# Optimization experiments

Hardware: AMD Instinct MI355X
Metric: run time of the kernel (lower is better)

The kernel has to match this reference:

```python
import jax, jax.numpy as jnp
import numpy as np

NUM_HEADS = 8
WINDOW = 128  # num_previous_frames
EPS = 1e-5


def setup_inputs() -> dict:
    key = jax.random.key(0)
    ks = jax.random.split(key, 5)
    B, T, E = 8, 1024, 512
    x = jax.random.normal(ks[0], (B, T, E), dtype=jnp.float32)
    x_lengths = jax.random.randint(ks[1], (B,), 1, T + 1).astype(jnp.int32)
    gamma = jnp.ones((E,), dtype=jnp.float32)
    beta = jnp.zeros((E,), dtype=jnp.float32)
    sc_in = 1.0 / np.sqrt(E)
    w_in = jax.random.normal(ks[2], (3 * E, E), dtype=jnp.float32) * sc_in
    b_in = jnp.zeros((3 * E,), dtype=jnp.float32)
    w_out = jax.random.normal(ks[3], (E, E), dtype=jnp.float32) * sc_in
    b_out = jnp.zeros((E,), dtype=jnp.float32)
    return {"x": x, "x_lengths": x_lengths, "gamma": gamma, "beta": beta,
            "w_in": w_in, "b_in": b_in, "w_out": w_out, "b_out": b_out}


def _forward(x, gamma, beta, w_in, b_in, w_out, b_out):
    B, T, E = x.shape
    H = NUM_HEADS
    D = E // H
    # Timewise LayerNorm: normalize over channel dim per (batch, time)
    mu = jnp.mean(x, axis=-1, keepdims=True)
    var = jnp.mean(jnp.square(x - mu), axis=-1, keepdims=True)
    xn = (x - mu) * jax.lax.rsqrt(var + EPS) * gamma + beta
    # in-projection: qkv packed
    qkv = xn @ w_in.T + b_in  # [B,T,3E]
    q, k, v = jnp.split(qkv, 3, axis=-1)
    q = q.reshape(B, T, H, D)
    k = k.reshape(B, T, H, D)
    v = v.reshape(B, T, H, D)
    scale = 1.0 / np.sqrt(D)
    scores = jnp.einsum('bqhd,bkhd->bhqk', q * scale, k)  # [B,H,T,T]
    # banded causal mask: allow j in [i-WINDOW, i]
    i = jnp.arange(T)[:, None]
    j = jnp.arange(T)[None, :]
    allowed = (j <= i) & (j >= i - WINDOW)
    scores = jnp.where(allowed[None, None], scores, -jnp.inf)
    attn = jax.nn.softmax(scores, axis=-1)
    ctx = jnp.einsum('bhqk,bkhd->bqhd', attn, v).reshape(B, T, E)
    out = ctx @ w_out.T + b_out
    return out  # dropout is identity in eval mode


def reference(x, x_lengths, gamma, beta, w_in, b_in, w_out, b_out):
    del x_lengths  # unused by the original forward (no key_padding_mask passed)
    return _forward(x, gamma, beta, w_in, b_in, w_out, b_out)
```

## Files before the change

kernel.cpp:

```cpp
#include <hip/hip_runtime.h>
#include <stdint.h>

typedef __bf16 bf16;
typedef __bf16 bf16x4 __attribute__((ext_vector_type(4)));
typedef __bf16 bf16x8 __attribute__((ext_vector_type(8)));
typedef float f32x4 __attribute__((ext_vector_type(4)));

#define MFMA_16x16x32(a, b, c) __builtin_amdgcn_mfma_f32_16x16x32_bf16((a), (b), (c), 0, 0, 0)

__device__ __forceinline__ void gl_lds16(const bf16* g, bf16* l) {
    __builtin_amdgcn_global_load_lds(
        (const __attribute__((address_space(1))) void*)g,
        (__attribute__((address_space(3))) void*)l, 16, 0, 0);
}

__global__ __launch_bounds__(256) void prep_kernel(const float* __restrict__ x,
                                                   const float* __restrict__ gamma,
                                                   const float* __restrict__ beta,
                                                   const float* __restrict__ w_in,
                                                   const float* __restrict__ w_out,
                                                   bf16* __restrict__ xn,
                                                   bf16* __restrict__ cw_in,
                                                   bf16* __restrict__ cw_out) {
    const int bid = blockIdx.x;
    if (bid < 2048) {
        const int lane = threadIdx.x & 63;
        const int row = (bid << 2) + (threadIdx.x >> 6);
        const size_t base = (size_t)row * 512 + lane * 8;
        const float* xf = x + base;
        float4 a = *(const float4*)xf;
        float4 b = *(const float4*)(xf + 4);
        float f[8] = {a.x, a.y, a.z, a.w, b.x, b.y, b.z, b.w};
        float s = 0.f;
#pragma unroll
        for (int j = 0; j < 8; ++j) s += f[j];
#pragma unroll
        for (int off = 32; off >= 1; off >>= 1) s += __shfl_xor(s, off, 64);
        const float mu = s * (1.0f / 512.0f);
        float vs = 0.f;
#pragma unroll
        for (int j = 0; j < 8; ++j) { float d = f[j] - mu; vs += d * d; }
#pragma unroll
        for (int off = 32; off >= 1; off >>= 1) vs += __shfl_xor(vs, off, 64);
        const float rstd = rsqrtf(vs * (1.0f / 512.0f) + 1e-5f);
        float4 g0 = *(const float4*)(gamma + lane * 8);
        float4 g1 = *(const float4*)(gamma + lane * 8 + 4);
        float4 b0 = *(const float4*)(beta + lane * 8);
        float4 b1 = *(const float4*)(beta + lane * 8 + 4);
        float gg[8] = {g0.x, g0.y, g0.z, g0.w, g1.x, g1.y, g1.z, g1.w};
        float bb[8] = {b0.x, b0.y, b0.z, b0.w, b1.x, b1.y, b1.z, b1.w};
        bf16x8 o;
#pragma unroll
        for (int j = 0; j < 8; ++j)
            o[j] = (bf16)((f[j] - mu) * rstd * gg[j] + bb[j]);
        *(bf16x8*)(xn + base) = o;
    } else {
        const float* src;
        bf16* dst;
        int base;
        if (bid < 2432) { src = w_in;  dst = cw_in;  base = (bid - 2048) * 2048; }
        else            { src = w_out; dst = cw_out; base = (bid - 2432) * 2048; }
        const int i = base + threadIdx.x * 8;
        float4 a = *(const float4*)(src + i);
        float4 b = *(const float4*)(src + i + 4);
        float f[8] = {a.x, a.y, a.z, a.w, b.x, b.y, b.z, b.w};
        bf16x8 o;
#pragma unroll
        for (int j = 0; j < 8; ++j) o[j] = (bf16)f[j];
        *(bf16x8*)(dst + i) = o;
    }
}

template <int TM, typename OT>
__global__ __launch_bounds__(256) void gemm_bt(const bf16* __restrict__ A,
                                               const bf16* __restrict__ B,
                                               const float* __restrict__ bias,
                                               OT* __restrict__ C,
                                               int N, int K) {
    constexpr int MI = TM / 32;
    constexpr int NCA = TM * 8;
    __shared__ alignas(16) bf16 As[TM * 64];
    __shared__ alignas(16) bf16 Bs[128 * 64];
    const int tid = threadIdx.x;
    const int lane = tid & 63;
    const int wid = tid >> 6;
    const int wm = (wid >> 1) * (TM / 2), wn = (wid & 1) * 64;
    const int m0 = blockIdx.y * TM, n0 = blockIdx.x * 128;
    const int l15 = lane & 15, l16 = lane >> 4;

    f32x4 acc[MI][4] = {};

    const bf16* Abase = A + (size_t)m0 * K;
    const bf16* Bbase = B + (size_t)n0 * K;

    for (int k0 = 0; k0 < K; k0 += 64) {
#pragma unroll
        for (int c = tid; c < NCA; c += 256) {
            const int p = c / (TM * 4);
            const int r = (c % (TM * 4)) >> 2;
            const int ko = (c & 3) * 8 + p * 32;
            gl_lds16(Abase + (size_t)r * K + k0 + ko, &As[c * 8]);
        }
#pragma unroll
        for (int c = tid; c < 1024; c += 256) {
            const int p = c >> 9;
            const int r = (c & 511) >> 2;
            const int ko = (c & 3) * 8 + p * 32;
            gl_lds16(Bbase + (size_t)r * K + k0 + ko, &Bs[c * 8]);
        }
        __syncthreads();
#pragma unroll
        for (int h = 0; h < 2; ++h) {
            bf16x8 af[MI], bfr[4];
#pragma unroll
            for (int t = 0; t < MI; ++t)
                af[t] = *(const bf16x8*)&As[h * (TM * 32) + (wm + t * 16 + l15) * 32 + l16 * 8];
#pragma unroll
            for (int t = 0; t < 4; ++t)
                bfr[t] = *(const bf16x8*)&Bs[h * 4096 + (wn + t * 16 + l15) * 32 + l16 * 8];
#pragma unroll
            for (int i = 0; i < MI; ++i)
#pragma unroll
                for (int j = 0; j < 4; ++j)
                    acc[i][j] = MFMA_16x16x32(bfr[j], af[i], acc[i][j]);
        }
        __syncthreads();
    }

#pragma unroll
    for (int j = 0; j < 4; ++j) {
        const int colb = n0 + wn + j * 16 + (l16 << 2);
        const float4 bv = *(const float4*)(bias + colb);
#pragma unroll
        for (int i = 0; i < MI; ++i) {
            const int row = m0 + wm + i * 16 + l15;
            if constexpr (sizeof(OT) == 2) {
                bf16x4 o;
                o[0] = (bf16)(acc[i][j][0] + bv.x);
                o[1] = (bf16)(acc[i][j][1] + bv.y);
                o[2] = (bf16)(acc[i][j][2] + bv.z);
                o[3] = (bf16)(acc[i][j][3] + bv.w);
                *(bf16x4*)&C[(size_t)row * N + colb] = o;
            } else {
                float4 o;
                o.x = acc[i][j][0] + bv.x;
                o.y = acc[i][j][1] + bv.y;
                o.z = acc[i][j][2] + bv.z;
                o.w = acc[i][j][3] + bv.w;
                *(float4*)&C[(size_t)row * N + colb] = o;
            }
        }
    }
}

#define KS_STRIDE 72
#define PW_STRIDE 72
#define VT_ROWB 400

__global__ __launch_bounds__(256) void attn_kernel(const bf16* __restrict__ qkv,
                                                   bf16* __restrict__ ctx) {
    __shared__ alignas(16) bf16 Ks[192 * KS_STRIDE];
    __shared__ alignas(16) char Vt[64 * VT_ROWB];
    __shared__ alignas(16) bf16 Pbuf[4 * 16 * PW_STRIDE];

    const int tid = threadIdx.x;
    const int lane = tid & 63, wid = tid >> 6;
    const int l15 = lane & 15, l16 = lane >> 4;
    const int bid = blockIdx.y * 16 + blockIdx.x;
    const int swz = (bid & 7) * 128 + (bid >> 3);
    const int bh = swz >> 4, b = bh >> 3, h = bh & 7;
    const int q0 = (swz & 15) * 64;
    const int kv0 = (q0 > 128) ? (q0 - 128) : 0;
    const int nk = q0 + 64 - kv0;
    const size_t tokbase = (size_t)b * 1024;

    for (int c = tid; c < nk * 8; c += 256) {
        const int kk = c >> 3, dc = (c & 7) * 8;
        const bf16* src = qkv + (tokbase + kv0 + kk) * 1536 + h * 64 + dc + 512;
        *(uint4*)&Ks[kk * KS_STRIDE + dc] = *(const uint4*)src;
    }
    for (int c = tid; c < nk * 4; c += 256) {
        const int kp = c >> 3, dc = (c & 7) * 8;
        const bf16* s0 = qkv + (tokbase + kv0 + 2 * kp) * 1536 + h * 64 + dc + 1024;
        uint4 w0 = *(const uint4*)s0;
        uint4 w1 = *(const uint4*)(s0 + 1536);
        const unsigned short* a0 = (const unsigned short*)&w0;
        const unsigned short* a1 = (const unsigned short*)&w1;
        const int u = kp >> 2, wb = (kp & 3) * 4;
#pragma unroll
        for (int j = 0; j < 8; ++j) {
            const int d = dc + j;
            *(uint*)&Vt[d * VT_ROWB + ((u ^ (d & 7)) << 4) + wb] =
                (uint)a0[j] | ((uint)a1[j] << 16);
        }
    }

    const int qt0 = q0 + wid * 16;
    const bf16* qptr = qkv + (tokbase + qt0 + l15) * 1536 + h * 64;
    bf16x8 qa0 = *(const bf16x8*)(qptr + l16 * 8);
    bf16x8 qa1 = *(const bf16x8*)(qptr + 32 + l16 * 8);

    __syncthreads();

    bf16* Pw = &Pbuf[wid * 16 * PW_STRIDE];
    f32x4 of[4] = {};
    float mst[4], lst[4];
#pragma unroll
    for (int r = 0; r < 4; ++r) { mst[r] = -1e30f; lst[r] = 0.f; }

    const int ktstart = ((qt0 > 128) ? (qt0 - 128) : 0) & ~63;
    for (int kt = ktstart; kt <= qt0 + 15; kt += 64) {
        const int krel = kt - kv0;
        int kgn = ((qt0 + 15 - kt) >> 4) + 1;
        if (kgn > 4) kgn = 4;
        const int dlo = qt0 - 128 - kt;
        const int kglo = (dlo > 0) ? (dlo >> 4) : 0;

        f32x4 s[4] = {};
        __builtin_amdgcn_s_setprio(1);
#pragma unroll
        for (int kg = 0; kg < 4; ++kg) {
            if (kg >= kglo && kg < kgn) {
                const bf16* kb = &Ks[(krel + kg * 16 + l15) * KS_STRIDE + l16 * 8];
                s[kg] = MFMA_16x16x32(qa0, *(const bf16x8*)kb, s[kg]);
                s[kg] = MFMA_16x16x32(qa1, *(const bf16x8*)(kb + 32), s[kg]);
            }
        }
        __builtin_amdgcn_s_setprio(0);

#pragma unroll
        for (int r = 0; r < 4; ++r) {
            const int qa = qt0 + l16 * 4 + r;
            float v[4];
#pragma unroll
            for (int kg = 0; kg < 4; ++kg) {
                const int key = kt + kg * 16 + l15;
                const bool ok = (key <= qa) && (key >= qa - 128);
                v[kg] = ok ? s[kg][r] * 0.125f : -1e30f;
            }
            float mx = fmaxf(fmaxf(v[0], v[1]), fmaxf(v[2], v[3]));
#pragma unroll
            for (int off = 1; off < 16; off <<= 1)
                mx = fmaxf(mx, __shfl_xor(mx, off, 64));
            const float mnew = fmaxf(mst[r], mx);
            const float alpha = __expf(mst[r] - mnew);
            const float e0 = __expf(v[0] - mnew);
            const float e1 = __expf(v[1] - mnew);
            const float e2 = __expf(v[2] - mnew);
            const float e3 = __expf(v[3] - mnew);
            float rs = (e0 + e1) + (e2 + e3);
#pragma unroll
            for (int off = 1; off < 16; off <<= 1)
                rs += __shfl_xor(rs, off, 64);
            lst[r] = lst[r] * alpha + rs;
            mst[r] = mnew;
#pragma unroll
            for (int nt = 0; nt < 4; ++nt) of[nt][r] *= alpha;
            const int q = l16 * 4 + r;
            Pw[q * PW_STRIDE + l15] = (bf16)e0;
            Pw[q * PW_STRIDE + 16 + l15] = (bf16)e1;
            Pw[q * PW_STRIDE + 32 + l15] = (bf16)e2;
            Pw[q * PW_STRIDE + 48 + l15] = (bf16)e3;
        }
        __asm__ volatile("s_waitcnt lgkmcnt(0)" ::: "memory");

        const bool haveA = (kglo < 2);
        const bool haveB = (kgn > 2);
        const int ub = krel >> 3;
        __builtin_amdgcn_s_setprio(1);
        if (haveA) {
            bf16x8 pa = *(const bf16x8*)&Pw[l15 * PW_STRIDE + l16 * 8];
#pragma unroll
            for (int nt = 0; nt < 4; ++nt) {
                const int d = nt * 16 + l15;
                bf16x8 vb = *(const bf16x8*)&Vt[d * VT_ROWB + (((ub + l16) ^ (d & 7)) << 4)];
                of[nt] = MFMA_16x16x32(pa, vb, of[nt]);
            }
        }
        if (haveB) {
            bf16x8 pa = *(const bf16x8*)&Pw[l15 * PW_STRIDE + 32 + l16 * 8];
#pragma unroll
            for (int nt = 0; nt < 4; ++nt) {
                const int d = nt * 16 + l15;
                bf16x8 vb = *(const bf16x8*)&Vt[d * VT_ROWB + (((ub + 4 + l16) ^ (d & 7)) << 4)];
                of[nt] = MFMA_16x16x32(pa, vb, of[nt]);
            }
        }
        __builtin_amdgcn_s_setprio(0);
    }

    float linv[4];
#pragma unroll
    for (int r = 0; r < 4; ++r) linv[r] = 1.0f / lst[r];
    bf16* cbase = ctx + (tokbase + qt0) * 512 + h * 64;
#pragma unroll
    for (int nt = 0; nt < 4; ++nt)
#pragma unroll
        for (int r = 0; r < 4; ++r) {
            const int q = l16 * 4 + r;
            cbase[(size_t)q * 512 + nt * 16 + l15] = (bf16)(of[nt][r] * linv[r]);
        }
}

extern "C" void kernel_launch(void* const* d_in, const int* in_sizes, int n_in,
                              void* d_out, int out_size, void* d_ws, size_t ws_size,
                              hipStream_t stream) {
    const float* x     = (const float*)d_in[0];
    const float* gamma = (const float*)d_in[2];
    const float* beta  = (const float*)d_in[3];
    const float* w_in  = (const float*)d_in[4];
    const float* b_in  = (const float*)d_in[5];
    const float* w_out = (const float*)d_in[6];
    const float* b_out = (const float*)d_in[7];
    float* out = (float*)d_out;

    char* ws = (char*)d_ws;
    bf16* cw_in  = (bf16*)ws;
    bf16* cw_out = cw_in + 786432;
    bf16* xn     = (bf16*)(ws + (4u << 20));
    bf16* qkv    = (bf16*)(ws + (12u << 20));
    bf16* ctx    = xn;

    prep_kernel<<<2560, 256, 0, stream>>>(x, gamma, beta, w_in, w_out, xn, cw_in, cw_out);
    gemm_bt<128, bf16><<<dim3(12, 64), 256, 0, stream>>>(xn, cw_in, b_in, qkv, 1536, 512);
    attn_kernel<<<dim3(16, 64), 256, 0, stream>>>(qkv, ctx);
    gemm_bt<64, float><<<dim3(4, 128), 256, 0, stream>>>(ctx, cw_out, b_out, out, 512, 512);
}
```

Measured before the change: 141.8 us.

## Swizzle attention LDS, lazily rescale softmax, halve P buffer, specialize GEMM K

The attention kernel moves from padded LDS strides to XOR-swizzled K and V tiles. It halves the per-wave P buffer by writing the second key half after the first PV MFMA, and requests 3 blocks per SM through launch bounds. Online softmax now rescales only when the running max grows by more than 8, which skips exp and accumulator multiplies. The masking test becomes a single unsigned compare, and the GEMM takes K as a template constant so its loop fully unrolls. The goal is less LDS per block, higher occupancy and fewer ALU ops, at the cost of extra LDS write/wait round trips and a bounded risk of float range growth from the deferred max.

```diff
diff --git a/kernel.cpp b/kernel.cpp
--- a/kernel.cpp
+++ b/kernel.cpp
@@ -71,12 +71,12 @@
     }
 }
 
-template <int TM, typename OT>
+template <int TM, int KK, typename OT>
 __global__ __launch_bounds__(256) void gemm_bt(const bf16* __restrict__ A,
                                                const bf16* __restrict__ B,
                                                const float* __restrict__ bias,
                                                OT* __restrict__ C,
-                                               int N, int K) {
+                                               int N) {
     constexpr int MI = TM / 32;
     constexpr int NCA = TM * 8;
     __shared__ alignas(16) bf16 As[TM * 64];
@@ -90,23 +90,24 @@
 
     f32x4 acc[MI][4] = {};
 
-    const bf16* Abase = A + (size_t)m0 * K;
-    const bf16* Bbase = B + (size_t)n0 * K;
-
-    for (int k0 = 0; k0 < K; k0 += 64) {
+    const bf16* Abase = A + (size_t)m0 * KK;
+    const bf16* Bbase = B + (size_t)n0 * KK;
+
+#pragma unroll
+    for (int k0 = 0; k0 < KK; k0 += 64) {
 #pragma unroll
         for (int c = tid; c < NCA; c += 256) {
             const int p = c / (TM * 4);
             const int r = (c % (TM * 4)) >> 2;
             const int ko = (c & 3) * 8 + p * 32;
-            gl_lds16(Abase + (size_t)r * K + k0 + ko, &As[c * 8]);
+            gl_lds16(Abase + (size_t)r * KK + k0 + ko, &As[c * 8]);
         }
 #pragma unroll
         for (int c = tid; c < 1024; c += 256) {
             const int p = c >> 9;
             const int r = (c & 511) >> 2;
             const int ko = (c & 3) * 8 + p * 32;
-            gl_lds16(Bbase + (size_t)r * K + k0 + ko, &Bs[c * 8]);
+            gl_lds16(Bbase + (size_t)r * KK + k0 + ko, &Bs[c * 8]);
         }
         __syncthreads();
 #pragma unroll
@@ -153,15 +154,11 @@
     }
 }
 
-#define KS_STRIDE 72
-#define PW_STRIDE 72
-#define VT_ROWB 400
-
-__global__ __launch_bounds__(256) void attn_kernel(const bf16* __restrict__ qkv,
-                                                   bf16* __restrict__ ctx) {
-    __shared__ alignas(16) bf16 Ks[192 * KS_STRIDE];
-    __shared__ alignas(16) char Vt[64 * VT_ROWB];
-    __shared__ alignas(16) bf16 Pbuf[4 * 16 * PW_STRIDE];
+__global__ __launch_bounds__(256, 3) void attn_kernel(const bf16* __restrict__ qkv,
+                                                      bf16* __restrict__ ctx) {
+    __shared__ alignas(16) bf16 Ks[192 * 64];
+    __shared__ alignas(16) char Vt[64 * 384];
+    __shared__ alignas(16) bf16 Pbuf[4 * 16 * 40];
 
     const int tid = threadIdx.x;
     const int lane = tid & 63, wid = tid >> 6;
@@ -175,9 +172,9 @@
     const size_t tokbase = (size_t)b * 1024;
 
     for (int c = tid; c < nk * 8; c += 256) {
-        const int kk = c >> 3, dc = (c & 7) * 8;
-        const bf16* src = qkv + (tokbase + kv0 + kk) * 1536 + h * 64 + dc + 512;
-        *(uint4*)&Ks[kk * KS_STRIDE + dc] = *(const uint4*)src;
+        const int kk = c >> 3, j = c & 7;
+        const bf16* src = qkv + (tokbase + kv0 + kk) * 1536 + h * 64 + j * 8 + 512;
+        *(uint4*)&Ks[kk * 64 + ((j ^ (kk & 7)) << 3)] = *(const uint4*)src;
     }
     for (int c = tid; c < nk * 4; c += 256) {
         const int kp = c >> 3, dc = (c & 7) * 8;
@@ -190,7 +187,7 @@
 #pragma unroll
         for (int j = 0; j < 8; ++j) {
             const int d = dc + j;
-            *(uint*)&Vt[d * VT_ROWB + ((u ^ (d & 7)) << 4) + wb] =
+            *(uint*)&Vt[d * 384 + ((u ^ (d & 7)) << 4) + wb] =
                 (uint)a0[j] | ((uint)a1[j] << 16);
         }
     }
@@ -202,7 +199,7 @@
 
     __syncthreads();
 
-    bf16* Pw = &Pbuf[wid * 16 * PW_STRIDE];
+    bf16* Pw = &Pbuf[wid * 16 * 40];
     f32x4 of[4] = {};
     float mst[4], lst[4];
 #pragma unroll
@@ -221,13 +218,18 @@
 #pragma unroll
         for (int kg = 0; kg < 4; ++kg) {
             if (kg >= kglo && kg < kgn) {
-                const bf16* kb = &Ks[(krel + kg * 16 + l15) * KS_STRIDE + l16 * 8];
-                s[kg] = MFMA_16x16x32(qa0, *(const bf16x8*)kb, s[kg]);
-                s[kg] = MFMA_16x16x32(qa1, *(const bf16x8*)(kb + 32), s[kg]);
+                const int row = krel + kg * 16 + l15;
+                const bf16* kb0 = &Ks[row * 64 + ((l16 ^ (row & 7)) << 3)];
+                const bf16* kb1 = &Ks[row * 64 + (((4 + l16) ^ (row & 7)) << 3)];
+                s[kg] = MFMA_16x16x32(qa0, *(const bf16x8*)kb0, s[kg]);
+                s[kg] = MFMA_16x16x32(qa1, *(const bf16x8*)kb1, s[kg]);
             }
         }
         __builtin_amdgcn_s_setprio(0);
 
+        const bool haveA = (kglo < 2);
+        const bool haveB = (kgn > 2);
+        float e2s[4], e3s[4];
 #pragma unroll
         for (int r = 0; r < 4; ++r) {
             const int qa = qt0 + l16 * 4 + r;
@@ -235,54 +237,62 @@
 #pragma unroll
             for (int kg = 0; kg < 4; ++kg) {
                 const int key = kt + kg * 16 + l15;
-                const bool ok = (key <= qa) && (key >= qa - 128);
-                v[kg] = ok ? s[kg][r] * 0.125f : -1e30f;
+                v[kg] = ((unsigned)(qa - key) <= 128u) ? s[kg][r] * 0.125f : -1e30f;
             }
             float mx = fmaxf(fmaxf(v[0], v[1]), fmaxf(v[2], v[3]));
 #pragma unroll
             for (int off = 1; off < 16; off <<= 1)
                 mx = fmaxf(mx, __shfl_xor(mx, off, 64));
-            const float mnew = fmaxf(mst[r], mx);
-            const float alpha = __expf(mst[r] - mnew);
-            const float e0 = __expf(v[0] - mnew);
-            const float e1 = __expf(v[1] - mnew);
-            const float e2 = __expf(v[2] - mnew);
-            const float e3 = __expf(v[3] - mnew);
+            if (__any(mx > mst[r] + 8.0f)) {
+                const float mnew = fmaxf(mst[r], mx);
+                const float alpha = __expf(mst[r] - mnew);
+                lst[r] *= alpha;
+#pragma unroll
+                for (int nt = 0; nt < 4; ++nt) of[nt][r] *= alpha;
+                mst[r] = mnew;
+            }
+            const float e0 = __expf(v[0] - mst[r]);
+            const float e1 = __expf(v[1] - mst[r]);
+            const float e2 = __expf(v[2] - mst[r]);
+            const float e3 = __expf(v[3] - mst[r]);
             float rs = (e0 + e1) + (e2 + e3);
 #pragma unroll
             for (int off = 1; off < 16; off <<= 1)
                 rs += __shfl_xor(rs, off, 64);
-            lst[r] = lst[r] * alpha + rs;
-            mst[r] = mnew;
-#pragma unroll
-            for (int nt = 0; nt < 4; ++nt) of[nt][r] *= alpha;
-            const int q = l16 * 4 + r;
-            Pw[q * PW_STRIDE + l15] = (bf16)e0;
-            Pw[q * PW_STRIDE + 16 + l15] = (bf16)e1;
-            Pw[q * PW_STRIDE + 32 + l15] = (bf16)e2;
-            Pw[q * PW_STRIDE + 48 + l15] = (bf16)e3;
-        }
-        __asm__ volatile("s_waitcnt lgkmcnt(0)" ::: "memory");
-
-        const bool haveA = (kglo < 2);
-        const bool haveB = (kgn > 2);
+            lst[r] += rs;
+            e2s[r] = e2; e3s[r] = e3;
+            if (haveA) {
+                const int q = l16 * 4 + r;
+                Pw[q * 40 + l15] = (bf16)e0;
+                Pw[q * 40 + 16 + l15] = (bf16)e1;
+            }
+        }
+
         const int ub = krel >> 3;
         __builtin_amdgcn_s_setprio(1);
         if (haveA) {
-            bf16x8 pa = *(const bf16x8*)&Pw[l15 * PW_STRIDE + l16 * 8];
+            __asm__ volatile("s_waitcnt lgkmcnt(0)" ::: "memory");
+            bf16x8 pa = *(const bf16x8*)&Pw[l15 * 40 + l16 * 8];
 #pragma unroll
             for (int nt = 0; nt < 4; ++nt) {
                 const int d = nt * 16 + l15;
-                bf16x8 vb = *(const bf16x8*)&Vt[d * VT_ROWB + (((ub + l16) ^ (d & 7)) << 4)];
+                bf16x8 vb = *(const bf16x8*)&Vt[d * 384 + (((ub + l16) ^ (d & 7)) << 4)];
                 of[nt] = MFMA_16x16x32(pa, vb, of[nt]);
             }
         }
         if (haveB) {
-            bf16x8 pa = *(const bf16x8*)&Pw[l15 * PW_STRIDE + 32 + l16 * 8];
+#pragma unroll
+            for (int r = 0; r < 4; ++r) {
+                const int q = l16 * 4 + r;
+                Pw[q * 40 + l15] = (bf16)e2s[r];
+                Pw[q * 40 + 16 + l15] = (bf16)e3s[r];
+            }
+            __asm__ volatile("s_waitcnt lgkmcnt(0)" ::: "memory");
+            bf16x8 pa = *(const bf16x8*)&Pw[l15 * 40 + l16 * 8];
 #pragma unroll
             for (int nt = 0; nt < 4; ++nt) {
                 const int d = nt * 16 + l15;
-                bf16x8 vb = *(const bf16x8*)&Vt[d * VT_ROWB + (((ub + 4 + l16) ^ (d & 7)) << 4)];
+                bf16x8 vb = *(const bf16x8*)&Vt[d * 384 + (((ub + 4 + l16) ^ (d & 7)) << 4)];
                 of[nt] = MFMA_16x16x32(pa, vb, of[nt]);
             }
         }
@@ -322,7 +332,7 @@
     bf16* ctx    = xn;
 
     prep_kernel<<<2560, 256, 0, stream>>>(x, gamma, beta, w_in, w_out, xn, cw_in, cw_out);
-    gemm_bt<128, bf16><<<dim3(12, 64), 256, 0, stream>>>(xn, cw_in, b_in, qkv, 1536, 512);
+    gemm_bt<128, 512, bf16><<<dim3(12, 64), 256, 0, stream>>>(xn, cw_in, b_in, qkv, 1536);
     attn_kernel<<<dim3(16, 64), 256, 0, stream>>>(qkv, ctx);
-    gemm_bt<64, float><<<dim3(4, 128), 256, 0, stream>>>(ctx, cw_out, b_out, out, 512, 512);
-}
+    gemm_bt<64, 512, float><<<dim3(4, 128), 256, 0, stream>>>(ctx, cw_out, b_out, out, 512);
+}
```

Measured after the change: 145.9 us. 2.9% more time.
